# Performance work log

Hardware: AMD Instinct MI355X
Metric: run time of the kernel (lower is better)

The kernel has to match this reference:

```python
import jax, jax.numpy as jnp
import numpy as np

N_NEURONS = 50000   # dense_shape[0]
N_INPUT = 17400     # dense_shape[1] (LGN units)
NNZ = 1_000_000     # number of sparse synapses
B, T = 1, 256       # batch, timesteps
BKG_SPIKE_RATE = 4  # hardcoded in original call()


def setup_inputs() -> dict:
    key = jax.random.key(0)
    k1, k2, k3, k4, k5 = jax.random.split(key, 5)
    rows = jax.random.randint(k1, (NNZ,), 0, N_NEURONS, dtype=jnp.int32)
    cols = jax.random.randint(k2, (NNZ,), 0, N_INPUT, dtype=jnp.int32)
    weights = jax.random.normal(k3, (NNZ,), dtype=jnp.float32)
    bkg_weights = jax.random.normal(k4, (N_NEURONS,), dtype=jnp.float32)
    inp = jax.random.uniform(k5, (B, T, N_INPUT), dtype=jnp.float32)
    return {"inp": inp, "weights": weights, "bkg_weights": bkg_weights,
            "rows": rows, "cols": cols}


def reference(inp, weights, bkg_weights, rows, cols):
    b, t, n_in = inp.shape
    x = inp.reshape(b * t, n_in)                     # (BT, n_input)
    # Sparse COO matmul: current[n, bt] = sum_{k: rows[k]==n} weights[k] * x[bt, cols[k]]
    # Equivalent to tf.sparse.sparse_dense_matmul(W_sparse, x, adjoint_b=True).
    contrib = weights[:, None] * x.T[cols]           # (nnz, BT)
    cur = jax.ops.segment_sum(contrib, rows, num_segments=N_NEURONS)  # (N, BT)
    cur = cur.T                                      # (BT, N) -- tf.transpose
    # Background noise: uniform(0,1) < 1 is always True, so rest == BKG_SPIKE_RATE.
    u = jax.random.uniform(jax.random.key(42), (b, t, BKG_SPIKE_RATE))
    rest = jnp.sum((u < 1.0).astype(inp.dtype), axis=-1)   # (b, t), constant 4
    noise = bkg_weights[None, None, :] * rest[..., None]   # (b, t, N)
    return cur.reshape(b, t, -1) + noise
```

## Files before the change

### kernel.cpp

```cpp
#include <hip/hip_runtime.h>

#define N_NEURONS 50000
#define N_INPUT   17400
#define NNZ_TOTAL 1000000
#define T_STEPS   256
#define ELL_CAP   64
#define GROUPS    8
#define ROWS_PER_GROUP 6250
#define BLKS_PER_GROUP 256
#define PER_BLK   3908

typedef float f4_t  __attribute__((ext_vector_type(4)));
typedef int   i4_t  __attribute__((ext_vector_type(4)));

__global__ __launch_bounds__(256) void transpose_kernel(
    const float* __restrict__ inp, ushort* __restrict__ xTb) {
    __shared__ float tile[32][33];
    const int bx = blockIdx.x;
    const int by = blockIdx.y;
    const int tx = threadIdx.x;
    const int ty = threadIdx.y;

    const int c = bx * 32 + tx;
#pragma unroll
    for (int i = 0; i < 4; ++i) {
        const int r = by * 32 + ty + i * 8;
        if (c < N_INPUT)
            tile[ty + i * 8][tx] = inp[r * N_INPUT + c];
    }
    __syncthreads();

    const int t = by * 32 + tx;
#pragma unroll
    for (int i = 0; i < 4; ++i) {
        const int rr = bx * 32 + ty + i * 8;
        if (rr < N_INPUT) {
            unsigned u = __float_as_uint(tile[tx][ty + i * 8]);
            u += 0x7fffu + ((u >> 16) & 1u);
            xTb[(size_t)rr * T_STEPS + t] = (ushort)(u >> 16);
        }
    }
}

__global__ __launch_bounds__(256) void ell_build_kernel(
    const int* __restrict__ rows, const int* __restrict__ cols,
    const float* __restrict__ w, int* __restrict__ cnt,
    unsigned* __restrict__ ell) {
    const int g    = blockIdx.x & (GROUPS - 1);
    const int blk  = blockIdx.x >> 3;
    const int r_lo = g * ROWS_PER_GROUP;
    const int r_hi = r_lo + ROWS_PER_GROUP;
    const int i_lo = blk * PER_BLK;
    const int i_hi = min(i_lo + PER_BLK, NNZ_TOTAL);

    for (int i = i_lo + (int)threadIdx.x * 4; i < i_hi; i += 256 * 4) {
        const i4_t r4 = __builtin_nontemporal_load((const i4_t*)&rows[i]);
        const i4_t c4 = __builtin_nontemporal_load((const i4_t*)&cols[i]);
        const f4_t w4 = __builtin_nontemporal_load((const f4_t*)&w[i]);
#pragma unroll
        for (int e = 0; e < 4; ++e) {
            const int r = r4[e];
            if (r >= r_lo && r < r_hi) {
                unsigned u = __float_as_uint(w4[e]);
                u += 0x7fffu + ((u >> 16) & 1u);
                const unsigned entry = ((unsigned)c4[e] << 16) | (u >> 16);
                const int p = atomicAdd(&cnt[r], 1);
                if (p < ELL_CAP)
                    ell[(size_t)r * ELL_CAP + p] = entry;
            }
        }
    }
}

__global__ __launch_bounds__(256) void spmm_kernel(
    const uint2* __restrict__ xT2,
    const int* __restrict__ cnt, const unsigned* __restrict__ ell,
    const float* __restrict__ bkg, float* __restrict__ out) {
    __shared__ float lds[16][260];
    const int tid  = threadIdx.x;
    const int lane = tid & 63;
    const int wv   = tid >> 6;
    const int base = blockIdx.x * 16;
    const int n0   = base + wv * 4;

    const int4   cv  = *(const int4*)&cnt[n0];
    const float4 bgv = *(const float4*)&bkg[n0];
    const int cs[4] = {min(cv.x, ELL_CAP), min(cv.y, ELL_CAP),
                       min(cv.z, ELL_CAP), min(cv.w, ELL_CAP)};
    const float bg[4] = {bgv.x, bgv.y, bgv.z, bgv.w};
    unsigned ev[4];
#pragma unroll
    for (int q = 0; q < 4; ++q) {
        const unsigned raw =
            __builtin_nontemporal_load(&ell[(size_t)(n0 + q) * ELL_CAP + lane]);
        ev[q] = (lane < cs[q]) ? raw : 0u;
    }

#pragma unroll
    for (int qq = 0; qq < 4; qq += 2) {
        const int cpad = (max(cs[qq], cs[qq + 1]) + 7) & ~7;
        float4 accA = make_float4(0.f, 0.f, 0.f, 0.f);
        float4 accB = make_float4(0.f, 0.f, 0.f, 0.f);

        for (int k0 = 0; k0 < cpad; k0 += 8) {
            unsigned eA[8], eB[8];
            uint2 xvA[8], xvB[8];
#pragma unroll
            for (int j = 0; j < 8; ++j) {
                eA[j] = __shfl(ev[qq],     k0 + j);
                eB[j] = __shfl(ev[qq + 1], k0 + j);
            }
#pragma unroll
            for (int j = 0; j < 8; ++j)
                xvA[j] = xT2[(size_t)(eA[j] >> 16) * 64 + lane];
#pragma unroll
            for (int j = 0; j < 8; ++j)
                xvB[j] = xT2[(size_t)(eB[j] >> 16) * 64 + lane];
#pragma unroll
            for (int j = 0; j < 8; ++j) {
                const float wk = __uint_as_float(eA[j] << 16);
                accA.x = fmaf(wk, __uint_as_float((xvA[j].x & 0xffffu) << 16), accA.x);
                accA.y = fmaf(wk, __uint_as_float(xvA[j].x & 0xffff0000u),     accA.y);
                accA.z = fmaf(wk, __uint_as_float((xvA[j].y & 0xffffu) << 16), accA.z);
                accA.w = fmaf(wk, __uint_as_float(xvA[j].y & 0xffff0000u),     accA.w);
            }
#pragma unroll
            for (int j = 0; j < 8; ++j) {
                const float wk = __uint_as_float(eB[j] << 16);
                accB.x = fmaf(wk, __uint_as_float((xvB[j].x & 0xffffu) << 16), accB.x);
                accB.y = fmaf(wk, __uint_as_float(xvB[j].x & 0xffff0000u),     accB.y);
                accB.z = fmaf(wk, __uint_as_float((xvB[j].y & 0xffffu) << 16), accB.z);
                accB.w = fmaf(wk, __uint_as_float(xvB[j].y & 0xffff0000u),     accB.w);
            }
        }
        const float bA = 4.0f * bg[qq];
        const float bB = 4.0f * bg[qq + 1];
        accA.x += bA; accA.y += bA; accA.z += bA; accA.w += bA;
        accB.x += bB; accB.y += bB; accB.z += bB; accB.w += bB;
        *(float4*)&lds[wv * 4 + qq][lane * 4]     = accA;
        *(float4*)&lds[wv * 4 + qq + 1][lane * 4] = accB;
    }
    __syncthreads();

    const int c4 = (tid & 3) * 4;
    const int t0 = tid >> 2;
#pragma unroll
    for (int t = t0; t < T_STEPS; t += 64) {
        f4_t v;
        v.x = lds[c4 + 0][t];
        v.y = lds[c4 + 1][t];
        v.z = lds[c4 + 2][t];
        v.w = lds[c4 + 3][t];
        __builtin_nontemporal_store(
            v, (f4_t*)&out[(size_t)t * N_NEURONS + base + c4]);
    }
}

extern "C" void kernel_launch(void* const* d_in, const int* in_sizes, int n_in,
                              void* d_out, int out_size, void* d_ws,
                              size_t ws_size, hipStream_t stream) {
    const float* inp     = (const float*)d_in[0];
    const float* weights = (const float*)d_in[1];
    const float* bkg     = (const float*)d_in[2];
    const int*   rows    = (const int*)d_in[3];
    const int*   cols    = (const int*)d_in[4];
    float*       out     = (float*)d_out;

    size_t off = 0;
    auto wsalloc = [&](size_t bytes) -> void* {
        void* p = (char*)d_ws + off;
        off += (bytes + 255) & ~size_t(255);
        return p;
    };
    ushort*   xTb = (ushort*)wsalloc(sizeof(ushort) * N_INPUT * T_STEPS);
    int*      cnt = (int*)wsalloc(sizeof(int) * N_NEURONS);
    unsigned* ell = (unsigned*)wsalloc(sizeof(unsigned) * N_NEURONS * ELL_CAP);
    (void)ws_size;

    (void)hipMemsetAsync(cnt, 0, sizeof(int) * N_NEURONS, stream);

    transpose_kernel<<<dim3((N_INPUT + 31) / 32, T_STEPS / 32), dim3(32, 8), 0,
                       stream>>>(inp, xTb);

    ell_build_kernel<<<GROUPS * BLKS_PER_GROUP, 256, 0, stream>>>(
        rows, cols, weights, cnt, ell);

    spmm_kernel<<<N_NEURONS / 16, 256, 0, stream>>>(
        (const uint2*)xTb, cnt, ell, bkg, out);
}
```

Before: 197.1 us.

## Merge transpose and ELL build into one launch; double-buffer SpMM gathers

Fuses the input transpose/bf16 conversion and the ELL construction into a single prep kernel, with block-index ranges selecting the role. This removes one launch and lets the two independent preprocessing stages run at the same time on the GPU. The SpMM inner loop is restructured into a two-stage software pipeline: the gathers for the next 8 entries are issued before the FMAs on the current 8. The cost is more live registers, which may reduce occupancy, and the weights are now re-shuffled in the FMA stage.

Result: no change. 196.8 us (-0.2%).

```diff
diff --git a/kernel.cpp b/kernel.cpp
--- a/kernel.cpp
+++ b/kernel.cpp
@@ -7,66 +7,68 @@
 #define ELL_CAP   64
 #define GROUPS    8
 #define ROWS_PER_GROUP 6250
-#define BLKS_PER_GROUP 256
+#define ELL_BLOCKS 2048
 #define PER_BLK   3908
+#define TP_TILES_X 544
+#define TP_BLOCKS (TP_TILES_X * 8)
 
 typedef float f4_t  __attribute__((ext_vector_type(4)));
 typedef int   i4_t  __attribute__((ext_vector_type(4)));
 
-__global__ __launch_bounds__(256) void transpose_kernel(
-    const float* __restrict__ inp, ushort* __restrict__ xTb) {
-    __shared__ float tile[32][33];
-    const int bx = blockIdx.x;
-    const int by = blockIdx.y;
-    const int tx = threadIdx.x;
-    const int ty = threadIdx.y;
-
-    const int c = bx * 32 + tx;
-#pragma unroll
-    for (int i = 0; i < 4; ++i) {
-        const int r = by * 32 + ty + i * 8;
-        if (c < N_INPUT)
-            tile[ty + i * 8][tx] = inp[r * N_INPUT + c];
-    }
-    __syncthreads();
-
-    const int t = by * 32 + tx;
-#pragma unroll
-    for (int i = 0; i < 4; ++i) {
-        const int rr = bx * 32 + ty + i * 8;
-        if (rr < N_INPUT) {
-            unsigned u = __float_as_uint(tile[tx][ty + i * 8]);
-            u += 0x7fffu + ((u >> 16) & 1u);
-            xTb[(size_t)rr * T_STEPS + t] = (ushort)(u >> 16);
-        }
-    }
-}
-
-__global__ __launch_bounds__(256) void ell_build_kernel(
+__global__ __launch_bounds__(256) void prep_kernel(
+    const float* __restrict__ inp, ushort* __restrict__ xTb,
     const int* __restrict__ rows, const int* __restrict__ cols,
     const float* __restrict__ w, int* __restrict__ cnt,
     unsigned* __restrict__ ell) {
-    const int g    = blockIdx.x & (GROUPS - 1);
-    const int blk  = blockIdx.x >> 3;
-    const int r_lo = g * ROWS_PER_GROUP;
-    const int r_hi = r_lo + ROWS_PER_GROUP;
-    const int i_lo = blk * PER_BLK;
-    const int i_hi = min(i_lo + PER_BLK, NNZ_TOTAL);
-
-    for (int i = i_lo + (int)threadIdx.x * 4; i < i_hi; i += 256 * 4) {
-        const i4_t r4 = __builtin_nontemporal_load((const i4_t*)&rows[i]);
-        const i4_t c4 = __builtin_nontemporal_load((const i4_t*)&cols[i]);
-        const f4_t w4 = __builtin_nontemporal_load((const f4_t*)&w[i]);
-#pragma unroll
-        for (int e = 0; e < 4; ++e) {
-            const int r = r4[e];
-            if (r >= r_lo && r < r_hi) {
-                unsigned u = __float_as_uint(w4[e]);
+    __shared__ float tile[32][33];
+    const int bid = blockIdx.x;
+
+    if (bid < ELL_BLOCKS) {
+        const int g    = bid & (GROUPS - 1);
+        const int blk  = bid >> 3;
+        const int r_lo = g * ROWS_PER_GROUP;
+        const int r_hi = r_lo + ROWS_PER_GROUP;
+        const int i_lo = blk * PER_BLK;
+        const int i_hi = min(i_lo + PER_BLK, NNZ_TOTAL);
+        for (int i = i_lo + (int)threadIdx.x * 4; i < i_hi; i += 256 * 4) {
+            const i4_t r4 = __builtin_nontemporal_load((const i4_t*)&rows[i]);
+            const i4_t c4 = __builtin_nontemporal_load((const i4_t*)&cols[i]);
+            const f4_t w4 = __builtin_nontemporal_load((const f4_t*)&w[i]);
+#pragma unroll
+            for (int e = 0; e < 4; ++e) {
+                const int r = r4[e];
+                if (r >= r_lo && r < r_hi) {
+                    unsigned u = __float_as_uint(w4[e]);
+                    u += 0x7fffu + ((u >> 16) & 1u);
+                    const unsigned entry = ((unsigned)c4[e] << 16) | (u >> 16);
+                    const int p = atomicAdd(&cnt[r], 1);
+                    if (p < ELL_CAP)
+                        ell[(size_t)r * ELL_CAP + p] = entry;
+                }
+            }
+        }
+    } else {
+        const int tb = bid - ELL_BLOCKS;
+        const int bx = tb % TP_TILES_X;
+        const int by = tb / TP_TILES_X;
+        const int tx = (int)threadIdx.x & 31;
+        const int ty = (int)threadIdx.x >> 5;
+        const int c = bx * 32 + tx;
+#pragma unroll
+        for (int i = 0; i < 4; ++i) {
+            const int r = by * 32 + ty + i * 8;
+            if (c < N_INPUT)
+                tile[ty + i * 8][tx] = inp[r * N_INPUT + c];
+        }
+        __syncthreads();
+        const int t = by * 32 + tx;
+#pragma unroll
+        for (int i = 0; i < 4; ++i) {
+            const int rr = bx * 32 + ty + i * 8;
+            if (rr < N_INPUT) {
+                unsigned u = __float_as_uint(tile[tx][ty + i * 8]);
                 u += 0x7fffu + ((u >> 16) & 1u);
-                const unsigned entry = ((unsigned)c4[e] << 16) | (u >> 16);
-                const int p = atomicAdd(&cnt[r], 1);
-                if (p < ELL_CAP)
-                    ell[(size_t)r * ELL_CAP + p] = entry;
+                xTb[(size_t)rr * T_STEPS + t] = (ushort)(u >> 16);
             }
         }
     }
@@ -98,41 +100,56 @@
 
 #pragma unroll
     for (int qq = 0; qq < 4; qq += 2) {
+        const unsigned ev0 = ev[qq];
+        const unsigned ev1 = ev[qq + 1];
         const int cpad = (max(cs[qq], cs[qq + 1]) + 7) & ~7;
         float4 accA = make_float4(0.f, 0.f, 0.f, 0.f);
         float4 accB = make_float4(0.f, 0.f, 0.f, 0.f);
 
-        for (int k0 = 0; k0 < cpad; k0 += 8) {
-            unsigned eA[8], eB[8];
-            uint2 xvA[8], xvB[8];
-#pragma unroll
-            for (int j = 0; j < 8; ++j) {
-                eA[j] = __shfl(ev[qq],     k0 + j);
-                eB[j] = __shfl(ev[qq + 1], k0 + j);
-            }
-#pragma unroll
-            for (int j = 0; j < 8; ++j)
-                xvA[j] = xT2[(size_t)(eA[j] >> 16) * 64 + lane];
-#pragma unroll
-            for (int j = 0; j < 8; ++j)
-                xvB[j] = xT2[(size_t)(eB[j] >> 16) * 64 + lane];
-#pragma unroll
-            for (int j = 0; j < 8; ++j) {
-                const float wk = __uint_as_float(eA[j] << 16);
-                accA.x = fmaf(wk, __uint_as_float((xvA[j].x & 0xffffu) << 16), accA.x);
-                accA.y = fmaf(wk, __uint_as_float(xvA[j].x & 0xffff0000u),     accA.y);
-                accA.z = fmaf(wk, __uint_as_float((xvA[j].y & 0xffffu) << 16), accA.z);
-                accA.w = fmaf(wk, __uint_as_float(xvA[j].y & 0xffff0000u),     accA.w);
-            }
-#pragma unroll
-            for (int j = 0; j < 8; ++j) {
-                const float wk = __uint_as_float(eB[j] << 16);
-                accB.x = fmaf(wk, __uint_as_float((xvB[j].x & 0xffffu) << 16), accB.x);
-                accB.y = fmaf(wk, __uint_as_float(xvB[j].x & 0xffff0000u),     accB.y);
-                accB.z = fmaf(wk, __uint_as_float((xvB[j].y & 0xffffu) << 16), accB.z);
-                accB.w = fmaf(wk, __uint_as_float(xvB[j].y & 0xffff0000u),     accB.w);
-            }
-        }
+        uint2 xa0[8], xb0[8], xa1[8], xb1[8];
+
+#define LOADB(XA, XB, K)                                                    \
+        {                                                                   \
+            _Pragma("unroll")                                               \
+            for (int j = 0; j < 8; ++j) {                                   \
+                const unsigned eA = __shfl(ev0, (K) + j);                   \
+                const unsigned eB = __shfl(ev1, (K) + j);                   \
+                XA[j] = xT2[(size_t)(eA >> 16) * 64 + lane];                \
+                XB[j] = xT2[(size_t)(eB >> 16) * 64 + lane];                \
+            }                                                               \
+        }
+
+#define FMAB(XA, XB, K)                                                     \
+        {                                                                   \
+            _Pragma("unroll")                                               \
+            for (int j = 0; j < 8; ++j) {                                   \
+                const float wA = __uint_as_float(__shfl(ev0, (K) + j) << 16); \
+                accA.x = fmaf(wA, __uint_as_float((XA[j].x & 0xffffu) << 16), accA.x); \
+                accA.y = fmaf(wA, __uint_as_float(XA[j].x & 0xffff0000u),     accA.y); \
+                accA.z = fmaf(wA, __uint_as_float((XA[j].y & 0xffffu) << 16), accA.z); \
+                accA.w = fmaf(wA, __uint_as_float(XA[j].y & 0xffff0000u),     accA.w); \
+                const float wB = __uint_as_float(__shfl(ev1, (K) + j) << 16); \
+                accB.x = fmaf(wB, __uint_as_float((XB[j].x & 0xffffu) << 16), accB.x); \
+                accB.y = fmaf(wB, __uint_as_float(XB[j].x & 0xffff0000u),     accB.y); \
+                accB.z = fmaf(wB, __uint_as_float((XB[j].y & 0xffffu) << 16), accB.z); \
+                accB.w = fmaf(wB, __uint_as_float(XB[j].y & 0xffff0000u),     accB.w); \
+            }                                                               \
+        }
+
+        LOADB(xa0, xb0, 0);
+        int k = 0;
+        while (k + 16 <= cpad) {
+            LOADB(xa1, xb1, k + 8);
+            FMAB(xa0, xb0, k);
+            if (k + 16 < cpad) LOADB(xa0, xb0, k + 16);
+            FMAB(xa1, xb1, k + 8);
+            k += 16;
+        }
+        if (k < cpad) FMAB(xa0, xb0, k);
+
+#undef LOADB
+#undef FMAB
+
         const float bA = 4.0f * bg[qq];
         const float bB = 4.0f * bg[qq + 1];
         accA.x += bA; accA.y += bA; accA.z += bA; accA.w += bA;
@@ -179,11 +196,8 @@
 
     (void)hipMemsetAsync(cnt, 0, sizeof(int) * N_NEURONS, stream);
 
-    transpose_kernel<<<dim3((N_INPUT + 31) / 32, T_STEPS / 32), dim3(32, 8), 0,
-                       stream>>>(inp, xTb);
-
-    ell_build_kernel<<<GROUPS * BLKS_PER_GROUP, 256, 0, stream>>>(
-        rows, cols, weights, cnt, ell);
+    prep_kernel<<<ELL_BLOCKS + TP_BLOCKS, 256, 0, stream>>>(
+        inp, xTb, rows, cols, weights, cnt, ell);
 
     spmm_kernel<<<N_NEURONS / 16, 256, 0, stream>>>(
         (const uint2*)xTb, cnt, ell, bkg, out);
```
